# Kernel optimization log

Hardware: AMD Instinct MI355X
Metric: run time of the kernel (lower is better)

The kernel has to match this reference:

```python
import jax, jax.numpy as jnp
import numpy as np

BS, DIM, EMB_DIM, SRC, TDEC, NEMB = 64, 512, 512, 400, 100, 50257


def intra_attention(h_t, h, W_attn):
    # h_t: [bs, dim]; h: [n, bs, dim]; W_attn: [dim, dim]
    n, bs, dim = h.shape
    # Faithful to torch .view([bs, dim, n]) on a contiguous [n, bs, dim]
    # tensor: raw row-major memory reinterpretation (NOT a transpose).
    hv = jnp.reshape(h, (bs, dim, n))  # [bs, dim, n]
    # E_t = (h_t @ W) [bs,1,dim] bmm hv [bs,dim,n] -> [bs, n]
    E = jnp.einsum('bd,bdn->bn', h_t @ W_attn, hv)
    # sum-normalized (non-softmax) score, eq. (4)
    A = E / jnp.sum(E, axis=1, keepdims=True)  # [bs, n]
    C = jnp.einsum('bdn,bn->bd', hv, A)        # [bs, dim]
    return A, C


def pointer_generator(ae_t, ce_t, hd_t, cd_t, W_emb, W_proj, W_u, b_u, b_out):
    # c_cat: [3*dim, bs]
    c_cat = jnp.concatenate((hd_t, ce_t, cd_t), axis=1).T
    # p_switch: [bs]
    p_switch = jax.nn.sigmoid(W_u @ c_cat + b_u).squeeze(0)
    # shared-embedding output projection, sect 2.4
    W_out = jnp.tanh(W_emb @ W_proj)           # [n_emb, 3*dim]
    logits = W_out @ c_cat + b_out             # [n_emb, bs]
    p_vocab = jax.nn.softmax(logits, axis=0)   # softmax over vocab
    p_gen = ((1.0 - p_switch) * p_vocab).T     # [bs, n_emb]
    p_copy = p_switch[:, None] * ae_t          # [bs, src]
    return p_gen, p_copy


def setup_inputs() -> dict:
    key = jax.random.key(0)
    ks = jax.random.split(key, 12)
    inp = {
        'h_t': jax.random.uniform(ks[0], (BS, DIM), dtype=jnp.float32),
        'h_enc': jax.random.uniform(ks[1], (SRC, BS, DIM), dtype=jnp.float32),
        'h_dec': jax.random.uniform(ks[2], (TDEC, BS, DIM), dtype=jnp.float32),
        'x': jax.random.randint(ks[3], (SRC, BS, 1), 0, NEMB, dtype=jnp.int64) if jax.config.jax_enable_x64 else jax.random.randint(ks[3], (SRC, BS, 1), 0, NEMB, dtype=jnp.int32),
        # positive attention weights keep the sum-normalized score well-conditioned
        'W_attn_enc': jax.random.uniform(ks[4], (DIM, DIM), dtype=jnp.float32, maxval=0.05),
        'W_attn_dec': jax.random.uniform(ks[5], (DIM, DIM), dtype=jnp.float32, maxval=0.05),
        'W_emb': jax.random.normal(ks[6], (NEMB, EMB_DIM), dtype=jnp.float32) * 0.02,
        'W_proj': jax.random.normal(ks[7], (EMB_DIM, 3 * DIM), dtype=jnp.float32) * 0.02,
        'W_u': jax.random.normal(ks[8], (1, 3 * DIM), dtype=jnp.float32) * 0.02,
        'b_u': jnp.zeros((1,), dtype=jnp.float32),
        'b_out': jnp.zeros((NEMB, 1), dtype=jnp.float32),
    }
    return inp


def reference(h_t, h_enc, h_dec, x, W_attn_enc, W_attn_dec, W_emb, W_proj, W_u, b_u, b_out):
    # one decode step of ReinforcedDecoder: enc attn + dec attn + pointer-gen
    ae_t, ce_t = intra_attention(h_t, h_enc, W_attn_enc)
    ad_t, cd_t = intra_attention(h_t, h_dec, W_attn_dec)
    p_gen, p_copy = pointer_generator(ae_t, ce_t, h_t, cd_t,
                                      W_emb, W_proj, W_u, b_u, b_out)
    return p_gen, p_copy
```

## Files before the change

### kernel.cpp

```cpp
#include <hip/hip_runtime.h>
#include <math.h>

typedef __attribute__((ext_vector_type(8))) short bf16x8;
typedef __attribute__((ext_vector_type(4))) float f32x4;
typedef __attribute__((ext_vector_type(4))) float f4v;

#define BS   64
#define DIM  512
#define SRC  400
#define TDEC 100
#define NEMB 50257
#define K3   1536

#define WS_Q     0
#define WS_EENC  65536
#define WS_EDEC  91136
#define WS_CENC  97536
#define WS_CDEC  130304
#define WS_ESUM  163072
#define WS_PSW   163200
#define WS_SMAX  163264
#define WS_SSUM  163328
#define WS_WPT   163392
#define WS_CCB   556608
#define WS_ZBEG  WS_CENC
#define WS_ZCNT  (WS_WPT - WS_CENC)

__device__ __forceinline__ ushort f2bf(float x) {
    union { float f; unsigned u; } v; v.f = x;
    unsigned r = (v.u + 0x7FFFu + ((v.u >> 16) & 1u)) >> 16;
    return (ushort)r;
}
__device__ __forceinline__ bf16x8 pack8v(f4v a, f4v b) {
    union { ushort us[8]; bf16x8 v; } p;
    p.us[0] = f2bf(a.x); p.us[1] = f2bf(a.y); p.us[2] = f2bf(a.z); p.us[3] = f2bf(a.w);
    p.us[4] = f2bf(b.x); p.us[5] = f2bf(b.y); p.us[6] = f2bf(b.z); p.us[7] = f2bf(b.w);
    return p.v;
}
__device__ __forceinline__ float pade_tanh(float x) {
    const float x2 = x * x;
    const float num = x * fmaf(x2, 1.0f / 15.0f, 1.0f);
    const float den = fmaf(x2, 0.4f, 1.0f);
    return num * __frcp_rn(den);
}
__device__ __forceinline__ unsigned fenc(float f) {
    unsigned b = __float_as_uint(f);
    return (b & 0x80000000u) ? ~b : (b | 0x80000000u);
}
__device__ __forceinline__ float fdec(unsigned k) {
    unsigned b = (k & 0x80000000u) ? (k & 0x7FFFFFFFu) : ~k;
    return __uint_as_float(b);
}
__device__ __forceinline__ void gl2lds16(const void* g, void* l) {
    __builtin_amdgcn_global_load_lds(
        (const __attribute__((address_space(1))) unsigned int*)g,
        (__attribute__((address_space(3))) unsigned int*)l, 16, 0, 0);
}

__global__ __launch_bounds__(256) void k_prep(const float* __restrict__ h_t,
                                              const float* __restrict__ Wenc,
                                              const float* __restrict__ Wdec,
                                              const float* __restrict__ Wp,
                                              float* __restrict__ ws) {
    __shared__ float sh[128 * 68];
    const int tid = threadIdx.x;
    if (blockIdx.x < 32) {
        const int which = blockIdx.x >> 4;
        const int c0 = (blockIdx.x & 15) * 32;
        const float* W = which ? Wdec : Wenc;
        float* q = ws + WS_Q + which * (BS * DIM);
        float* hS = sh;
        float* WSm = sh + 64 * 65;
        const int c = tid & 31, bg = tid >> 5;
        float acc[8] = {0.f, 0.f, 0.f, 0.f, 0.f, 0.f, 0.f, 0.f};
        for (int kc = 0; kc < 8; ++kc) {
            __syncthreads();
            #pragma unroll
            for (int r = 0; r < 16; ++r) {
                const int idx = r * 256 + tid;
                const int b = idx >> 6, k = idx & 63;
                hS[b * 65 + k] = h_t[b * DIM + kc * 64 + k];
            }
            #pragma unroll
            for (int r = 0; r < 8; ++r) {
                const int idx = r * 256 + tid;
                const int k = idx >> 5, cc = idx & 31;
                WSm[k * 33 + cc] = W[(size_t)(kc * 64 + k) * DIM + c0 + cc];
            }
            __syncthreads();
            #pragma unroll 8
            for (int k = 0; k < 64; ++k) {
                const float wv = WSm[k * 33 + c];
                #pragma unroll
                for (int bb = 0; bb < 8; ++bb)
                    acc[bb] = fmaf(hS[(bg * 8 + bb) * 65 + k], wv, acc[bb]);
            }
        }
        #pragma unroll
        for (int bb = 0; bb < 8; ++bb)
            q[(bg * 8 + bb) * DIM + c0 + c] = acc[bb];
    } else {
        const int bid = blockIdx.x - 32;
        const int t = bid >> 2, c = bid & 3;
        float (*T32)[68] = (float (*)[68])sh;
        #pragma unroll
        for (int p = 0; p < 8; ++p) {
            const int idx = p * 256 + tid;
            const int kk = idx >> 4, s = idx & 15;
            const float4 v = *(const float4*)(Wp + (size_t)(c * 128 + kk) * K3 + t * 64 + s * 4);
            T32[kk][s * 4 + 0] = v.x; T32[kk][s * 4 + 1] = v.y;
            T32[kk][s * 4 + 2] = v.z; T32[kk][s * 4 + 3] = v.w;
        }
        __syncthreads();
        char* dst = (char*)(ws + WS_WPT) + (size_t)bid * 16384;
        #pragma unroll
        for (int p = 0; p < 4; ++p) {
            const int fid = p * 256 + tid;
            const int lane = fid & 63;
            const int J = (fid >> 6) & 3;
            const int ks = fid >> 8;
            const int j = J * 16 + (lane & 15);
            const int k0 = ks * 32 + (lane >> 4) * 8;
            f4v a, b;
            a.x = T32[k0 + 0][j]; a.y = T32[k0 + 1][j];
            a.z = T32[k0 + 2][j]; a.w = T32[k0 + 3][j];
            b.x = T32[k0 + 4][j]; b.y = T32[k0 + 5][j];
            b.z = T32[k0 + 6][j]; b.w = T32[k0 + 7][j];
            *(bf16x8*)(dst + fid * 16) = pack8v(a, b);
        }
    }
}

#define IC 16
__global__ __launch_bounds__(256) void k_attn(const float* __restrict__ h_enc,
                                              const float* __restrict__ h_dec,
                                              float* __restrict__ ws) {
    const int b = blockIdx.x, which = blockIdx.y, z = blockIdx.z;
    const int tid = threadIdx.x;
    const int n   = which ? TDEC : SRC;
    const int per = which ? (TDEC / 4) : (SRC / 4);
    const int i_begin = z * per, i_end = i_begin + per;
    const float* h  = which ? h_dec : h_enc;
    const float* q  = ws + WS_Q + which * (BS * DIM) + b * DIM;
    float* wsE      = ws + (which ? WS_EDEC : WS_EENC) + b * n;
    float* Cws      = ws + (which ? WS_CDEC : WS_CENC) + b * DIM;
    const float* hb = h + (size_t)b * DIM * n;

    __shared__ float hS[DIM * (IC + 1)];
    __shared__ float qs[DIM];
    __shared__ float Ered[256];
    __shared__ float Es[IC];

    qs[tid] = q[tid];
    qs[tid + 256] = q[tid + 256];

    const int ii = tid & (IC - 1);
    const int dg = tid >> 4;
    float c0 = 0.f, c1 = 0.f, esum = 0.f;

    for (int i0 = i_begin; i0 < i_end; i0 += IC) {
        const int ic = min(IC, i_end - i0);
        __syncthreads();
        #pragma unroll 8
        for (int idx = tid; idx < DIM * IC; idx += 256) {
            const int d = idx >> 4, i = idx & (IC - 1);
            hS[d * (IC + 1) + i] = (i < ic) ? hb[(size_t)d * n + i0 + i] : 0.f;
        }
        __syncthreads();
        float p = 0.f;
        #pragma unroll 8
        for (int d = dg * 32; d < dg * 32 + 32; ++d) p += qs[d] * hS[d * (IC + 1) + ii];
        Ered[dg * IC + ii] = p;
        __syncthreads();
        if (tid < IC) {
            float e = 0.f;
            #pragma unroll
            for (int g = 0; g < 16; ++g) e += Ered[g * IC + tid];
            Es[tid] = e;
            esum += e;
            if (tid < ic) wsE[i0 + tid] = e;
        }
        __syncthreads();
        #pragma unroll
        for (int i = 0; i < IC; ++i) {
            const float e = Es[i];
            c0 += hS[tid * (IC + 1) + i] * e;
            c1 += hS[(tid + 256) * (IC + 1) + i] * e;
        }
    }
    atomicAdd(&Cws[tid], c0);
    atomicAdd(&Cws[tid + 256], c1);
    __syncthreads();
    if (tid < IC) Ered[tid] = esum;
    __syncthreads();
    if (tid == 0) {
        float s = 0.f;
        #pragma unroll
        for (int g = 0; g < IC; ++g) s += Ered[g];
        atomicAdd(&ws[WS_ESUM + which * 64 + b], s);
    }
}

__global__ void k_pswitch(const float* __restrict__ h_t,
                          const float* __restrict__ W_u,
                          const float* __restrict__ b_u,
                          float* __restrict__ out_copy,
                          float* __restrict__ ws) {
    const int b = blockIdx.x, tid = threadIdx.x;
    const float invE = 1.f / ws[WS_ESUM + b];
    const float invD = 1.f / ws[WS_ESUM + 64 + b];
    const float* Ce = ws + WS_CENC + b * DIM;
    const float* Cd = ws + WS_CDEC + b * DIM;
    ushort* ccB = (ushort*)(ws + WS_CCB);
    __shared__ float red[256];
    float part = 0.f;
    #pragma unroll
    for (int r = 0; r < 6; ++r) {
        const int j = tid + r * 256;
        float v = (j < DIM) ? h_t[b * DIM + j]
                            : ((j < 2 * DIM) ? Ce[j - DIM] * invE : Cd[j - 2 * DIM] * invD);
        ccB[(size_t)b * K3 + j] = f2bf(v);
        part += W_u[j] * v;
    }
    red[tid] = part;
    __syncthreads();
    for (int s = 128; s > 0; s >>= 1) {
        if (tid < s) red[tid] += red[tid + s];
        __syncthreads();
    }
    const float ps = 1.f / (1.f + expf(-(red[0] + b_u[0])));
    if (tid == 0) ws[WS_PSW + b] = ps;
    const float* Ee = ws + WS_EENC + b * SRC;
    for (int i = tid; i < SRC; i += 256) out_copy[b * SRC + i] = ps * Ee[i] * invE;
}

#define VB 64
__global__ __launch_bounds__(256, 2) void k_bigmm(const float* __restrict__ We,
                                                  const float* __restrict__ ws,
                                                  const float* __restrict__ b_out,
                                                  float* __restrict__ out) {
    __shared__ __align__(16) char smem[57344];
    const ushort* ccB = (const ushort*)(ws + WS_CCB);
    const char* wptb  = (const char*)(ws + WS_WPT);

    const int tid  = threadIdx.x;
    const int w    = tid >> 6, lane = tid & 63;
    const int lrow = lane & 15, lgrp = lane >> 4;
    const int vw   = blockIdx.x * VB + w * 16;
    const int row  = vw + lrow;
    char* tbase = smem + 49152 + w * 2048;
    const int swz = (lrow & 7) << 4;

    #pragma unroll
    for (int p = 0; p < 3; ++p) {
        const char* src = wptb + (size_t)p * 16384 + tid * 16;
        char* dst = smem + p * 16384 + tid * 16;
        #pragma unroll
        for (int rnd = 0; rnd < 4; ++rnd) gl2lds16(src + rnd * 4096, dst + rnd * 4096);
    }

    bf16x8 A[16];
    if (row < NEMB) {
        const f4v* p = (const f4v*)(We + (size_t)row * DIM + lgrp * 8);
        #pragma unroll
        for (int f = 0; f < 16; ++f) {
            const f4v x0 = __builtin_nontemporal_load(p + f * 8);
            const f4v x1 = __builtin_nontemporal_load(p + f * 8 + 1);
            A[f] = pack8v(x0, x1);
        }
    } else {
        #pragma unroll
        for (int f = 0; f < 16; ++f) A[f] = (bf16x8){0, 0, 0, 0, 0, 0, 0, 0};
    }

    f32x4 La[4], Ta[4];
    #pragma unroll
    for (int i = 0; i < 4; ++i) {
        La[i] = (f32x4){0.f, 0.f, 0.f, 0.f};
        Ta[i] = (f32x4){0.f, 0.f, 0.f, 0.f};
    }

    for (int it = 0; it < 8; ++it) {
        #pragma unroll
        for (int u = 0; u < 12; ++u) {
            const int i = it * 12 + u;
            asm volatile("s_waitcnt vmcnt(8)" ::: "memory");
            __builtin_amdgcn_s_barrier();
            {
                const char* bp = smem + (u % 3) * 16384 + lane * 16;
                #pragma unroll
                for (int ks = 0; ks < 4; ++ks) {
                    const bf16x8 b0 = *(const bf16x8*)(bp + ks * 4096);
                    const bf16x8 b1 = *(const bf16x8*)(bp + ks * 4096 + 1024);
                    const bf16x8 b2 = *(const bf16x8*)(bp + ks * 4096 + 2048);
                    const bf16x8 b3 = *(const bf16x8*)(bp + ks * 4096 + 3072);
                    Ta[0] = __builtin_amdgcn_mfma_f32_16x16x32_bf16(A[(u & 3) * 4 + ks], b0, Ta[0], 0, 0, 0);
                    Ta[1] = __builtin_amdgcn_mfma_f32_16x16x32_bf16(A[(u & 3) * 4 + ks], b1, Ta[1], 0, 0, 0);
                    Ta[2] = __builtin_amdgcn_mfma_f32_16x16x32_bf16(A[(u & 3) * 4 + ks], b2, Ta[2], 0, 0, 0);
                    Ta[3] = __builtin_amdgcn_mfma_f32_16x16x32_bf16(A[(u & 3) * 4 + ks], b3, Ta[3], 0, 0, 0);
                }
            }
            if ((u & 3) == 3) {
                const int t = it * 3 + (u >> 2);
                #pragma unroll
                for (int nj = 0; nj < 4; ++nj) {
                    const int j = nj * 16 + lrow;
                    #pragma unroll
                    for (int r = 0; r < 4; ++r) {
                        const int v = lgrp * 4 + r;
                        *(ushort*)(tbase + v * 128 + ((j * 2) ^ ((v & 7) << 4))) =
                            f2bf(pade_tanh(Ta[nj][r]));
                    }
                }
                #pragma unroll
                for (int kc = 0; kc < 2; ++kc) {
                    const bf16x8 tf = *(const bf16x8*)(tbase + lrow * 128 +
                                                       ((kc * 64 + lgrp * 16) ^ swz));
                    const ushort* cc = ccB + (size_t)lrow * K3 + t * 64 + kc * 32 + lgrp * 8;
                    const bf16x8 c0 = *(const bf16x8*)(cc);
                    const bf16x8 c1 = *(const bf16x8*)(cc + 16 * K3);
                    const bf16x8 c2 = *(const bf16x8*)(cc + 32 * K3);
                    const bf16x8 c3 = *(const bf16x8*)(cc + 48 * K3);
                    La[0] = __builtin_amdgcn_mfma_f32_16x16x32_bf16(tf, c0, La[0], 0, 0, 0);
                    La[1] = __builtin_amdgcn_mfma_f32_16x16x32_bf16(tf, c1, La[1], 0, 0, 0);
                    La[2] = __builtin_amdgcn_mfma_f32_16x16x32_bf16(tf, c2, La[2], 0, 0, 0);
                    La[3] = __builtin_amdgcn_mfma_f32_16x16x32_bf16(tf, c3, La[3], 0, 0, 0);
                }
                #pragma unroll
                for (int z = 0; z < 4; ++z) Ta[z] = (f32x4){0.f, 0.f, 0.f, 0.f};
            }
            __builtin_amdgcn_s_barrier();
            if (i + 3 < 96) {
                const char* src = wptb + (size_t)(i + 3) * 16384 + tid * 16;
                char* dst = smem + (u % 3) * 16384 + tid * 16;
                #pragma unroll
                for (int rnd = 0; rnd < 4; ++rnd)
                    gl2lds16(src + rnd * 4096, dst + rnd * 4096);
            }
        }
    }

    #pragma unroll
    for (int nb = 0; nb < 4; ++nb) {
        const int b = nb * 16 + lrow;
        #pragma unroll
        for (int r = 0; r < 4; ++r) {
            const int v = vw + lgrp * 4 + r;
            if (v < NEMB) out[(size_t)b * NEMB + v] = La[nb][r] + b_out[v];
        }
    }
}

#define VC 12565
__global__ void k_colmax(const float* __restrict__ out, float* __restrict__ ws) {
    const int b = blockIdx.x, vc = blockIdx.y, tid = threadIdx.x;
    const float* L = out + (size_t)b * NEMB;
    const int vend = min((vc + 1) * VC, NEMB);
    float m = -1e30f;
    for (int v = vc * VC + tid; v < vend; v += 256) m = fmaxf(m, L[v]);
    __shared__ float red[256];
    red[tid] = m;
    __syncthreads();
    for (int s = 128; s > 0; s >>= 1) {
        if (tid < s) red[tid] = fmaxf(red[tid], red[tid + s]);
        __syncthreads();
    }
    if (tid == 0) atomicMax((unsigned*)(ws + WS_SMAX) + b, fenc(red[0]));
}

__global__ void k_colsum(const float* __restrict__ out, float* __restrict__ ws) {
    const int b = blockIdx.x, vc = blockIdx.y, tid = threadIdx.x;
    const float* L = out + (size_t)b * NEMB;
    const float mb = fdec(((const unsigned*)(ws + WS_SMAX))[b]);
    const int vend = min((vc + 1) * VC, NEMB);
    float sum = 0.f;
    for (int v = vc * VC + tid; v < vend; v += 256) sum += expf(L[v] - mb);
    __shared__ float red[256];
    red[tid] = sum;
    __syncthreads();
    for (int s = 128; s > 0; s >>= 1) {
        if (tid < s) red[tid] += red[tid + s];
        __syncthreads();
    }
    if (tid == 0) atomicAdd(ws + WS_SSUM + b, red[0]);
}

__global__ void k_finalize(float* __restrict__ out, const float* __restrict__ ws) {
    const int total = BS * NEMB;
    const int stride = gridDim.x * blockDim.x;
    for (int idx = blockIdx.x * blockDim.x + threadIdx.x; idx < total; idx += stride) {
        const int b = idx / NEMB;
        const float mb = fdec(((const unsigned*)(ws + WS_SMAX))[b]);
        const float sb = ws[WS_SSUM + b];
        const float ps = ws[WS_PSW + b];
        out[idx] = (1.f - ps) * expf(out[idx] - mb) / sb;
    }
}

extern "C" void kernel_launch(void* const* d_in, const int* in_sizes, int n_in,
                              void* d_out, int out_size, void* d_ws, size_t ws_size,
                              hipStream_t stream) {
    const float* h_t        = (const float*)d_in[0];
    const float* h_enc      = (const float*)d_in[1];
    const float* h_dec      = (const float*)d_in[2];
    const float* W_attn_enc = (const float*)d_in[4];
    const float* W_attn_dec = (const float*)d_in[5];
    const float* W_emb      = (const float*)d_in[6];
    const float* W_proj     = (const float*)d_in[7];
    const float* W_u        = (const float*)d_in[8];
    const float* b_u        = (const float*)d_in[9];
    const float* b_out      = (const float*)d_in[10];

    float* out = (float*)d_out;
    float* ws  = (float*)d_ws;
    float* out_copy = out + (size_t)BS * NEMB;

    hipMemsetAsync(ws + WS_ZBEG, 0, (size_t)WS_ZCNT * sizeof(float), stream);
    k_prep   <<<128, 256, 0, stream>>>(h_t, W_attn_enc, W_attn_dec, W_proj, ws);
    k_attn   <<<dim3(64, 2, 4), 256, 0, stream>>>(h_enc, h_dec, ws);
    k_pswitch<<<64, 256, 0, stream>>>(h_t, W_u, b_u, out_copy, ws);
    k_bigmm  <<<(NEMB + VB - 1) / VB, 256, 0, stream>>>(W_emb, ws, b_out, out);
    k_colmax <<<dim3(64, 4), 256, 0, stream>>>(out, ws);
    k_colsum <<<dim3(64, 4), 256, 0, stream>>>(out, ws);
    k_finalize<<<4096, 256, 0, stream>>>(out, ws);
}
```

Measured before the change: 366.6 us.

## Double vocab rows per warp in bigmm and fuse softmax into one kernel

Each warp in the main GEMM now handles 32 vocab rows instead of 16, so every W_proj tile staged in LDS and every ccB fragment feeds twice as many MFMAs, and the grid is halved. The wait counts are adjusted near the end of the pipeline. The three softmax passes (colmax, colsum, finalize), which used atomics across kernels, are replaced by a single kernel with one 1024-thread block per batch row, which removes two launches and the atomic workspace traffic. The cost is higher register pressure in bigmm, and the softmax now runs on only 64 blocks, which may underuse the GPU.

```diff
diff --git a/kernel.cpp b/kernel.cpp
--- a/kernel.cpp
+++ b/kernel.cpp
@@ -42,14 +42,6 @@
     const float num = x * fmaf(x2, 1.0f / 15.0f, 1.0f);
     const float den = fmaf(x2, 0.4f, 1.0f);
     return num * __frcp_rn(den);
-}
-__device__ __forceinline__ unsigned fenc(float f) {
-    unsigned b = __float_as_uint(f);
-    return (b & 0x80000000u) ? ~b : (b | 0x80000000u);
-}
-__device__ __forceinline__ float fdec(unsigned k) {
-    unsigned b = (k & 0x80000000u) ? (k & 0x7FFFFFFFu) : ~k;
-    return __uint_as_float(b);
 }
 __device__ __forceinline__ void gl2lds16(const void* g, void* l) {
     __builtin_amdgcn_global_load_lds(
@@ -234,21 +226,22 @@
     for (int i = tid; i < SRC; i += 256) out_copy[b * SRC + i] = ps * Ee[i] * invE;
 }
 
-#define VB 64
+#define VB 128
+#define WAITV(N) asm volatile("s_waitcnt vmcnt(" #N ")" ::: "memory")
 __global__ __launch_bounds__(256, 2) void k_bigmm(const float* __restrict__ We,
                                                   const float* __restrict__ ws,
                                                   const float* __restrict__ b_out,
                                                   float* __restrict__ out) {
-    __shared__ __align__(16) char smem[57344];
+    __shared__ __align__(16) char smem[65536];
     const ushort* ccB = (const ushort*)(ws + WS_CCB);
     const char* wptb  = (const char*)(ws + WS_WPT);
 
     const int tid  = threadIdx.x;
     const int w    = tid >> 6, lane = tid & 63;
     const int lrow = lane & 15, lgrp = lane >> 4;
-    const int vw   = blockIdx.x * VB + w * 16;
-    const int row  = vw + lrow;
-    char* tbase = smem + 49152 + w * 2048;
+    const int vw   = blockIdx.x * VB + w * 32;
+    const int row0 = vw + lrow, row1 = vw + 16 + lrow;
+    char* tbase = smem + 49152 + w * 4096;
     const int swz = (lrow & 7) << 4;
 
     #pragma unroll
@@ -259,32 +252,42 @@
         for (int rnd = 0; rnd < 4; ++rnd) gl2lds16(src + rnd * 4096, dst + rnd * 4096);
     }
 
-    bf16x8 A[16];
-    if (row < NEMB) {
-        const f4v* p = (const f4v*)(We + (size_t)row * DIM + lgrp * 8);
-        #pragma unroll
-        for (int f = 0; f < 16; ++f) {
-            const f4v x0 = __builtin_nontemporal_load(p + f * 8);
-            const f4v x1 = __builtin_nontemporal_load(p + f * 8 + 1);
-            A[f] = pack8v(x0, x1);
-        }
+    bf16x8 A0[16], A1[16];
+    if (row0 < NEMB) {
+        const f4v* p = (const f4v*)(We + (size_t)row0 * DIM + lgrp * 8);
+        #pragma unroll
+        for (int f = 0; f < 16; ++f)
+            A0[f] = pack8v(__builtin_nontemporal_load(p + f * 8),
+                           __builtin_nontemporal_load(p + f * 8 + 1));
     } else {
         #pragma unroll
-        for (int f = 0; f < 16; ++f) A[f] = (bf16x8){0, 0, 0, 0, 0, 0, 0, 0};
-    }
-
-    f32x4 La[4], Ta[4];
+        for (int f = 0; f < 16; ++f) A0[f] = (bf16x8){0, 0, 0, 0, 0, 0, 0, 0};
+    }
+    if (row1 < NEMB) {
+        const f4v* p = (const f4v*)(We + (size_t)row1 * DIM + lgrp * 8);
+        #pragma unroll
+        for (int f = 0; f < 16; ++f)
+            A1[f] = pack8v(__builtin_nontemporal_load(p + f * 8),
+                           __builtin_nontemporal_load(p + f * 8 + 1));
+    } else {
+        #pragma unroll
+        for (int f = 0; f < 16; ++f) A1[f] = (bf16x8){0, 0, 0, 0, 0, 0, 0, 0};
+    }
+
+    f32x4 La0[4], La1[4], Ta0[4], Ta1[4];
     #pragma unroll
     for (int i = 0; i < 4; ++i) {
-        La[i] = (f32x4){0.f, 0.f, 0.f, 0.f};
-        Ta[i] = (f32x4){0.f, 0.f, 0.f, 0.f};
+        La0[i] = (f32x4){0.f, 0.f, 0.f, 0.f}; La1[i] = (f32x4){0.f, 0.f, 0.f, 0.f};
+        Ta0[i] = (f32x4){0.f, 0.f, 0.f, 0.f}; Ta1[i] = (f32x4){0.f, 0.f, 0.f, 0.f};
     }
 
     for (int it = 0; it < 8; ++it) {
         #pragma unroll
         for (int u = 0; u < 12; ++u) {
             const int i = it * 12 + u;
-            asm volatile("s_waitcnt vmcnt(8)" ::: "memory");
+            if (u == 10)      { if (it == 7) WAITV(4); else WAITV(8); }
+            else if (u == 11) { if (it == 7) WAITV(0); else WAITV(8); }
+            else              { WAITV(8); }
             __builtin_amdgcn_s_barrier();
             {
                 const char* bp = smem + (u % 3) * 16384 + lane * 16;
@@ -294,10 +297,14 @@
                     const bf16x8 b1 = *(const bf16x8*)(bp + ks * 4096 + 1024);
                     const bf16x8 b2 = *(const bf16x8*)(bp + ks * 4096 + 2048);
                     const bf16x8 b3 = *(const bf16x8*)(bp + ks * 4096 + 3072);
-                    Ta[0] = __builtin_amdgcn_mfma_f32_16x16x32_bf16(A[(u & 3) * 4 + ks], b0, Ta[0], 0, 0, 0);
-                    Ta[1] = __builtin_amdgcn_mfma_f32_16x16x32_bf16(A[(u & 3) * 4 + ks], b1, Ta[1], 0, 0, 0);
-                    Ta[2] = __builtin_amdgcn_mfma_f32_16x16x32_bf16(A[(u & 3) * 4 + ks], b2, Ta[2], 0, 0, 0);
-                    Ta[3] = __builtin_amdgcn_mfma_f32_16x16x32_bf16(A[(u & 3) * 4 + ks], b3, Ta[3], 0, 0, 0);
+                    Ta0[0] = __builtin_amdgcn_mfma_f32_16x16x32_bf16(A0[(u & 3) * 4 + ks], b0, Ta0[0], 0, 0, 0);
+                    Ta1[0] = __builtin_amdgcn_mfma_f32_16x16x32_bf16(A1[(u & 3) * 4 + ks], b0, Ta1[0], 0, 0, 0);
+                    Ta0[1] = __builtin_amdgcn_mfma_f32_16x16x32_bf16(A0[(u & 3) * 4 + ks], b1, Ta0[1], 0, 0, 0);
+                    Ta1[1] = __builtin_amdgcn_mfma_f32_16x16x32_bf16(A1[(u & 3) * 4 + ks], b1, Ta1[1], 0, 0, 0);
+                    Ta0[2] = __builtin_amdgcn_mfma_f32_16x16x32_bf16(A0[(u & 3) * 4 + ks], b2, Ta0[2], 0, 0, 0);
+                    Ta1[2] = __builtin_amdgcn_mfma_f32_16x16x32_bf16(A1[(u & 3) * 4 + ks], b2, Ta1[2], 0, 0, 0);
+                    Ta0[3] = __builtin_amdgcn_mfma_f32_16x16x32_bf16(A0[(u & 3) * 4 + ks], b3, Ta0[3], 0, 0, 0);
+                    Ta1[3] = __builtin_amdgcn_mfma_f32_16x16x32_bf16(A1[(u & 3) * 4 + ks], b3, Ta1[3], 0, 0, 0);
                 }
             }
             if ((u & 3) == 3) {
@@ -309,25 +316,36 @@
                     for (int r = 0; r < 4; ++r) {
                         const int v = lgrp * 4 + r;
                         *(ushort*)(tbase + v * 128 + ((j * 2) ^ ((v & 7) << 4))) =
-                            f2bf(pade_tanh(Ta[nj][r]));
+                            f2bf(pade_tanh(Ta0[nj][r]));
+                        *(ushort*)(tbase + (16 + v) * 128 + ((j * 2) ^ ((v & 7) << 4))) =
+                            f2bf(pade_tanh(Ta1[nj][r]));
                     }
                 }
                 #pragma unroll
                 for (int kc = 0; kc < 2; ++kc) {
-                    const bf16x8 tf = *(const bf16x8*)(tbase + lrow * 128 +
-                                                       ((kc * 64 + lgrp * 16) ^ swz));
+                    const bf16x8 tf0 = *(const bf16x8*)(tbase + lrow * 128 +
+                                                        ((kc * 64 + lgrp * 16) ^ swz));
+                    const bf16x8 tf1 = *(const bf16x8*)(tbase + (16 + lrow) * 128 +
+                                                        ((kc * 64 + lgrp * 16) ^ swz));
                     const ushort* cc = ccB + (size_t)lrow * K3 + t * 64 + kc * 32 + lgrp * 8;
                     const bf16x8 c0 = *(const bf16x8*)(cc);
                     const bf16x8 c1 = *(const bf16x8*)(cc + 16 * K3);
                     const bf16x8 c2 = *(const bf16x8*)(cc + 32 * K3);
                     const bf16x8 c3 = *(const bf16x8*)(cc + 48 * K3);
-                    La[0] = __builtin_amdgcn_mfma_f32_16x16x32_bf16(tf, c0, La[0], 0, 0, 0);
-                    La[1] = __builtin_amdgcn_mfma_f32_16x16x32_bf16(tf, c1, La[1], 0, 0, 0);
-                    La[2] = __builtin_amdgcn_mfma_f32_16x16x32_bf16(tf, c2, La[2], 0, 0, 0);
-                    La[3] = __builtin_amdgcn_mfma_f32_16x16x32_bf16(tf, c3, La[3], 0, 0, 0);
+                    La0[0] = __builtin_amdgcn_mfma_f32_16x16x32_bf16(tf0, c0, La0[0], 0, 0, 0);
+                    La1[0] = __builtin_amdgcn_mfma_f32_16x16x32_bf16(tf1, c0, La1[0], 0, 0, 0);
+                    La0[1] = __builtin_amdgcn_mfma_f32_16x16x32_bf16(tf0, c1, La0[1], 0, 0, 0);
+                    La1[1] = __builtin_amdgcn_mfma_f32_16x16x32_bf16(tf1, c1, La1[1], 0, 0, 0);
+                    La0[2] = __builtin_amdgcn_mfma_f32_16x16x32_bf16(tf0, c2, La0[2], 0, 0, 0);
+                    La1[2] = __builtin_amdgcn_mfma_f32_16x16x32_bf16(tf1, c2, La1[2], 0, 0, 0);
+                    La0[3] = __builtin_amdgcn_mfma_f32_16x16x32_bf16(tf0, c3, La0[3], 0, 0, 0);
+                    La1[3] = __builtin_amdgcn_mfma_f32_16x16x32_bf16(tf1, c3, La1[3], 0, 0, 0);
                 }
                 #pragma unroll
-                for (int z = 0; z < 4; ++z) Ta[z] = (f32x4){0.f, 0.f, 0.f, 0.f};
+                for (int z = 0; z < 4; ++z) {
+                    Ta0[z] = (f32x4){0.f, 0.f, 0.f, 0.f};
+                    Ta1[z] = (f32x4){0.f, 0.f, 0.f, 0.f};
+                }
             }
             __builtin_amdgcn_s_barrier();
             if (i + 3 < 96) {
@@ -345,56 +363,39 @@
         const int b = nb * 16 + lrow;
         #pragma unroll
         for (int r = 0; r < 4; ++r) {
-            const int v = vw + lgrp * 4 + r;
-            if (v < NEMB) out[(size_t)b * NEMB + v] = La[nb][r] + b_out[v];
-        }
-    }
-}
-
-#define VC 12565
-__global__ void k_colmax(const float* __restrict__ out, float* __restrict__ ws) {
-    const int b = blockIdx.x, vc = blockIdx.y, tid = threadIdx.x;
-    const float* L = out + (size_t)b * NEMB;
-    const int vend = min((vc + 1) * VC, NEMB);
+            const int v0 = vw + lgrp * 4 + r;
+            const int v1 = v0 + 16;
+            if (v0 < NEMB) out[(size_t)b * NEMB + v0] = La0[nb][r] + b_out[v0];
+            if (v1 < NEMB) out[(size_t)b * NEMB + v1] = La1[nb][r] + b_out[v1];
+        }
+    }
+}
+
+__global__ __launch_bounds__(1024) void k_softmax(float* __restrict__ out,
+                                                  const float* __restrict__ ws) {
+    const int b = blockIdx.x, tid = threadIdx.x;
+    float* L = out + (size_t)b * NEMB;
+    __shared__ float red[1024];
     float m = -1e30f;
-    for (int v = vc * VC + tid; v < vend; v += 256) m = fmaxf(m, L[v]);
-    __shared__ float red[256];
+    for (int v = tid; v < NEMB; v += 1024) m = fmaxf(m, L[v]);
     red[tid] = m;
     __syncthreads();
-    for (int s = 128; s > 0; s >>= 1) {
+    for (int s = 512; s > 0; s >>= 1) {
         if (tid < s) red[tid] = fmaxf(red[tid], red[tid + s]);
         __syncthreads();
     }
-    if (tid == 0) atomicMax((unsigned*)(ws + WS_SMAX) + b, fenc(red[0]));
-}
-
-__global__ void k_colsum(const float* __restrict__ out, float* __restrict__ ws) {
-    const int b = blockIdx.x, vc = blockIdx.y, tid = threadIdx.x;
-    const float* L = out + (size_t)b * NEMB;
-    const float mb = fdec(((const unsigned*)(ws + WS_SMAX))[b]);
-    const int vend = min((vc + 1) * VC, NEMB);
+    const float mb = red[0];
+    __syncthreads();
     float sum = 0.f;
-    for (int v = vc * VC + tid; v < vend; v += 256) sum += expf(L[v] - mb);
-    __shared__ float red[256];
+    for (int v = tid; v < NEMB; v += 1024) sum += expf(L[v] - mb);
     red[tid] = sum;
     __syncthreads();
-    for (int s = 128; s > 0; s >>= 1) {
+    for (int s = 512; s > 0; s >>= 1) {
         if (tid < s) red[tid] += red[tid + s];
         __syncthreads();
     }
-    if (tid == 0) atomicAdd(ws + WS_SSUM + b, red[0]);
-}
-
-__global__ void k_finalize(float* __restrict__ out, const float* __restrict__ ws) {
-    const int total = BS * NEMB;
-    const int stride = gridDim.x * blockDim.x;
-    for (int idx = blockIdx.x * blockDim.x + threadIdx.x; idx < total; idx += stride) {
-        const int b = idx / NEMB;
-        const float mb = fdec(((const unsigned*)(ws + WS_SMAX))[b]);
-        const float sb = ws[WS_SSUM + b];
-        const float ps = ws[WS_PSW + b];
-        out[idx] = (1.f - ps) * expf(out[idx] - mb) / sb;
-    }
+    const float scale = (1.f - ws[WS_PSW + b]) / red[0];
+    for (int v = tid; v < NEMB; v += 1024) L[v] = expf(L[v] - mb) * scale;
 }
 
 extern "C" void kernel_launch(void* const* d_in, const int* in_sizes, int n_in,
@@ -420,7 +421,5 @@
     k_attn   <<<dim3(64, 2, 4), 256, 0, stream>>>(h_enc, h_dec, ws);
     k_pswitch<<<64, 256, 0, stream>>>(h_t, W_u, b_u, out_copy, ws);
     k_bigmm  <<<(NEMB + VB - 1) / VB, 256, 0, stream>>>(W_emb, ws, b_out, out);
-    k_colmax <<<dim3(64, 4), 256, 0, stream>>>(out, ws);
-    k_colsum <<<dim3(64, 4), 256, 0, stream>>>(out, ws);
-    k_finalize<<<4096, 256, 0, stream>>>(out, ws);
-}
+    k_softmax<<<64, 1024, 0, stream>>>(out, ws);
+}
```

Result: faster. 339.0 us (-7.5%).
